# Kernel optimization log

Hardware: AMD Instinct MI355X
Metric: run time of the kernel (lower is better)

## Reference

```python
import jax, jax.numpy as jnp
import numpy as np

N_NODES = 50000
N_EDGES = 600000
D_OBJ = 128
D_REL = 128
D_OUT = 128


def setup_inputs() -> dict:
    key = jax.random.key(0)
    ks = jax.random.split(key, 7)
    s_obj = 1.0 / np.sqrt(D_OBJ)
    s_rel = 1.0 / np.sqrt(D_REL)
    return {
        "obj_vecs": jax.random.normal(ks[0], (N_NODES, D_OBJ), dtype=jnp.float32),
        "rel_vecs": jax.random.normal(ks[1], (N_EDGES, D_REL), dtype=jnp.float32),
        "edge_index": jax.random.randint(ks[2], (N_EDGES, 2), 0, N_NODES, dtype=jnp.int64),
        "W_obj": jax.random.normal(ks[3], (D_OUT, D_OBJ), dtype=jnp.float32) * s_obj,
        "b_obj": jax.random.normal(ks[4], (D_OUT,), dtype=jnp.float32) * s_obj,
        "W_rel": jax.random.normal(ks[5], (D_OUT, D_REL), dtype=jnp.float32) * s_rel,
        "b_rel": jax.random.normal(ks[6], (D_OUT,), dtype=jnp.float32) * s_rel,
    }


def reference(obj_vecs, rel_vecs, edge_index, W_obj, b_obj, W_rel, b_rel):
    # Per-node linear once ([N, d_out]) instead of twice per edge -- same math
    # since lin_obj(x_i) + lin_obj(x_j) = (x_i W^T + b) + (x_j W^T + b).
    obj_lin = obj_vecs @ W_obj.T + b_obj            # [N, d_out]
    rel_lin = rel_vecs @ W_rel.T + b_rel            # [E, d_out]
    src = edge_index[:, 0]
    dst = edge_index[:, 1]
    # message = relu(lin_obj(obj_i) + lin_rel(rel_k) + lin_obj(obj_j))
    msg = jax.nn.relu(obj_lin[src] + rel_lin + obj_lin[dst])  # [E, d_out]
    # aggr='add', flow source_to_target: scatter-add at target nodes (col 1)
    aggr = jax.ops.segment_sum(msg, dst, num_segments=obj_vecs.shape[0])
    return jax.nn.relu(aggr)
```

## Files before the change

kernel.cpp:

```cpp
#include <hip/hip_runtime.h>

#define N_NODES 50000
#define N_EDGES 600000
#define DD 128

typedef __attribute__((ext_vector_type(8))) short short8;
typedef __attribute__((ext_vector_type(4))) float f32x4;

__device__ __forceinline__ short f2bf(float f) {
    union { float f; unsigned u; } v; v.f = f;
    unsigned r = v.u + 0x7fffu + ((v.u >> 16) & 1u);
    return (short)(r >> 16);
}
__device__ __forceinline__ float bf2f(short s) {
    union { float f; unsigned u; } v; v.u = ((unsigned)(unsigned short)s) << 16;
    return v.f;
}
__device__ __forceinline__ float u2f(unsigned u) {
    union { float f; unsigned u; } v; v.u = u;
    return v.f;
}

__global__ __launch_bounds__(256) void k_lin(const float* __restrict__ X,
                                             const float* __restrict__ W,
                                             const float* __restrict__ bias,
                                             short* __restrict__ Y,
                                             int ntiles) {
    __shared__ __align__(16) short Wf[128 * 128];
    for (int i = threadIdx.x; i < 2048; i += 256) {
        const int fl = i & 63, fr = i >> 6;
        const int nt = fr >> 2, ks = fr & 3, fg = fl >> 4, fln = fl & 15;
        const float* s = W + (nt * 16 + fln) * DD + ks * 32 + fg * 8;
        short* d = Wf + i * 8;
#pragma unroll
        for (int j = 0; j < 8; ++j) d[j] = f2bf(s[j]);
    }
    __syncthreads();

    const int wave = threadIdx.x >> 6;
    const int lane = threadIdx.x & 63;
    const int g = lane >> 4, ln = lane & 15;

    float bb[8];
#pragma unroll
    for (int nt = 0; nt < 8; ++nt) bb[nt] = bias[nt * 16 + ln];

    for (int t = blockIdx.x * 4 + wave; t < ntiles; t += gridDim.x * 4) {
        const float* xr = X + (size_t)(t * 16 + ln) * DD;
        short8 a[4];
#pragma unroll
        for (int ks = 0; ks < 4; ++ks) {
            const float* p = xr + ks * 32 + g * 8;
            float4 t0 = *(const float4*)p;
            float4 t1 = *(const float4*)(p + 4);
            short8 v;
            v[0] = f2bf(t0.x); v[1] = f2bf(t0.y); v[2] = f2bf(t0.z); v[3] = f2bf(t0.w);
            v[4] = f2bf(t1.x); v[5] = f2bf(t1.y); v[6] = f2bf(t1.z); v[7] = f2bf(t1.w);
            a[ks] = v;
        }
#pragma unroll
        for (int nt = 0; nt < 8; ++nt) {
            f32x4 acc = {0.f, 0.f, 0.f, 0.f};
#pragma unroll
            for (int ks = 0; ks < 4; ++ks) {
                short8 b = *(const short8*)(Wf + (((nt << 2) + ks) * 64 + lane) * 8);
                acc = __builtin_amdgcn_mfma_f32_16x16x32_bf16(a[ks], b, acc, 0, 0, 0);
            }
#pragma unroll
            for (int r = 0; r < 4; ++r)
                Y[(size_t)(t * 16 + g * 4 + r) * DD + nt * 16 + ln] = f2bf(acc[r] + bb[nt]);
        }
    }
}

__global__ __launch_bounds__(256) void k_zero_int(int* __restrict__ p, int n) {
    int i = blockIdx.x * 256 + threadIdx.x;
    if (i < n) p[i] = 0;
}

__global__ __launch_bounds__(256) void k_count(const int* __restrict__ EI,
                                               int* __restrict__ counts) {
    int e = blockIdx.x * 256 + threadIdx.x;
    if (e < N_EDGES) atomicAdd(&counts[EI[2 * e + 1]], 1);
}

__global__ __launch_bounds__(256) void k_scan1(const int* __restrict__ counts,
                                               int* __restrict__ scanned,
                                               int* __restrict__ bsum) {
    __shared__ int tmp[256];
    const int t = threadIdx.x;
    const int i = blockIdx.x * 256 + t;
    int v = (i < N_NODES) ? counts[i] : 0;
    tmp[t] = v;
    __syncthreads();
#pragma unroll
    for (int off = 1; off < 256; off <<= 1) {
        int x = (t >= off) ? tmp[t - off] : 0;
        __syncthreads();
        tmp[t] += x;
        __syncthreads();
    }
    if (i < N_NODES) scanned[i] = tmp[t] - v;
    if (t == 255) bsum[blockIdx.x] = tmp[255];
}

__global__ __launch_bounds__(256) void k_scan2(int* __restrict__ bsum, int nb) {
    __shared__ int tmp[256];
    const int t = threadIdx.x;
    int v = (t < nb) ? bsum[t] : 0;
    tmp[t] = v;
    __syncthreads();
#pragma unroll
    for (int off = 1; off < 256; off <<= 1) {
        int x = (t >= off) ? tmp[t - off] : 0;
        __syncthreads();
        tmp[t] += x;
        __syncthreads();
    }
    if (t < nb) bsum[t] = tmp[t] - v;
}

__global__ __launch_bounds__(256) void k_scan3(const int* __restrict__ scanned,
                                               const int* __restrict__ bsum,
                                               int* __restrict__ offsets,
                                               int* __restrict__ cursor) {
    int i = blockIdx.x * 256 + threadIdx.x;
    if (i < N_NODES) {
        int off = scanned[i] + bsum[blockIdx.x];
        offsets[i] = off;
        cursor[i] = off;
    }
    if (i == 0) offsets[N_NODES] = N_EDGES;
}

__global__ __launch_bounds__(256) void k_scatter2(const int* __restrict__ EI,
                                                  int* __restrict__ cursor,
                                                  int* __restrict__ perm) {
    int e = blockIdx.x * 256 + threadIdx.x;
    if (e < N_EDGES)
        perm[e] = atomicAdd(&cursor[EI[2 * e + 1]], 1);
}

__global__ __launch_bounds__(256) void k_fl(const float* __restrict__ RV,
                                            const int* __restrict__ EI,
                                            const int* __restrict__ perm,
                                            const float* __restrict__ W,
                                            const float* __restrict__ bias,
                                            const short* __restrict__ OL,
                                            unsigned short* __restrict__ Ys) {
    __shared__ __align__(16) short Wf[128 * 128];
    __shared__ __align__(16) unsigned stg[4][1160];

    for (int i = threadIdx.x; i < 2048; i += 256) {
        const int fl = i & 63, fr = i >> 6;
        const int nt = fr >> 2, ks = fr & 3, fg = fl >> 4, fln = fl & 15;
        const float* s = W + (nt * 16 + fln) * DD + ks * 32 + fg * 8;
        short* d = Wf + i * 8;
#pragma unroll
        for (int j = 0; j < 8; ++j) d[j] = f2bf(s[j]);
    }
    __syncthreads();

    const int wave = threadIdx.x >> 6;
    const int lane = threadIdx.x & 63;
    const int g = lane >> 4, ln = lane & 15;
    unsigned* st = stg[wave];

    const float br0 = bias[lane];
    const float br1 = bias[lane + 64];
    const unsigned short* OLu = (const unsigned short*)OL;
    const int NT = N_EDGES / 16;

    for (int t = blockIdx.x * 4 + wave; t < NT; t += gridDim.x * 4) {
        const int e0 = t * 16;

        const float* xr = RV + (size_t)(e0 + ln) * DD;
        short8 a[4];
#pragma unroll
        for (int ks = 0; ks < 4; ++ks) {
            const float* p = xr + ks * 32 + g * 8;
            float4 t0 = *(const float4*)p;
            float4 t1 = *(const float4*)(p + 4);
            short8 v;
            v[0] = f2bf(t0.x); v[1] = f2bf(t0.y); v[2] = f2bf(t0.z); v[3] = f2bf(t0.w);
            v[4] = f2bf(t1.x); v[5] = f2bf(t1.y); v[6] = f2bf(t1.z); v[7] = f2bf(t1.w);
            a[ks] = v;
        }

        int sp = 0, pp = 0;
        if (lane < 16) {
            sp = EI[2 * (e0 + lane)];
            pp = perm[e0 + lane];
        }

        f32x4 acc[8];
#pragma unroll
        for (int nt = 0; nt < 8; ++nt) {
            acc[nt] = (f32x4){0.f, 0.f, 0.f, 0.f};
#pragma unroll
            for (int ks = 0; ks < 4; ++ks) {
                short8 b = *(const short8*)(Wf + (((nt << 2) + ks) * 64 + lane) * 8);
                acc[nt] = __builtin_amdgcn_mfma_f32_16x16x32_bf16(a[ks], b, acc[nt], 0, 0, 0);
            }
        }

#pragma unroll
        for (int nt = 0; nt < 8; ++nt) {
            const unsigned lo = ((unsigned)(unsigned short)f2bf(acc[nt][0])) |
                                (((unsigned)(unsigned short)f2bf(acc[nt][1])) << 16);
            const unsigned hi = ((unsigned)(unsigned short)f2bf(acc[nt][2])) |
                                (((unsigned)(unsigned short)f2bf(acc[nt][3])) << 16);
            const int c = nt * 16 + ln;
            st[c * 9 + g * 2]     = lo;
            st[c * 9 + g * 2 + 1] = hi;
        }

#pragma unroll 4
        for (int e = 0; e < 16; ++e) {
            const int src = __shfl(sp, e);
            const int pos = __shfl(pp, e);
            const unsigned w0 = st[lane * 9 + (e >> 1)];
            const unsigned w1 = st[(lane + 64) * 9 + (e >> 1)];
            const float s0 = (e & 1) ? u2f(w0 & 0xffff0000u) : u2f(w0 << 16);
            const float s1 = (e & 1) ? u2f(w1 & 0xffff0000u) : u2f(w1 << 16);
            const float y0 = s0 + br0 + bf2f((short)OLu[(size_t)src * DD + lane]);
            const float y1 = s1 + br1 + bf2f((short)OLu[(size_t)src * DD + lane + 64]);
            Ys[(size_t)pos * DD + lane]      = (unsigned short)f2bf(y0);
            Ys[(size_t)pos * DD + lane + 64] = (unsigned short)f2bf(y1);
        }
    }
}

__global__ __launch_bounds__(256) void k_segsum(const unsigned short* __restrict__ Ys,
                                                const short* __restrict__ OL,
                                                const int* __restrict__ offs,
                                                float* __restrict__ out) {
    const int wave = threadIdx.x >> 6;
    const int lane = threadIdx.x & 63;
    const int v = blockIdx.x * 4 + wave;
    if (v >= N_NODES) return;

    const int r0 = offs[v], r1 = offs[v + 1];
    const unsigned short* OLu = (const unsigned short*)OL;
    const float od0 = bf2f((short)OLu[(size_t)v * DD + lane]);
    const float od1 = bf2f((short)OLu[(size_t)v * DD + lane + 64]);

    float a0 = 0.f, a1 = 0.f;
    int r = r0;
    for (; r + 2 <= r1; r += 2) {
        const float y00 = bf2f((short)Ys[(size_t)r * DD + lane]);
        const float y01 = bf2f((short)Ys[(size_t)r * DD + lane + 64]);
        const float y10 = bf2f((short)Ys[(size_t)(r + 1) * DD + lane]);
        const float y11 = bf2f((short)Ys[(size_t)(r + 1) * DD + lane + 64]);
        a0 += fmaxf(y00 + od0, 0.f) + fmaxf(y10 + od0, 0.f);
        a1 += fmaxf(y01 + od1, 0.f) + fmaxf(y11 + od1, 0.f);
    }
    if (r < r1) {
        a0 += fmaxf(bf2f((short)Ys[(size_t)r * DD + lane]) + od0, 0.f);
        a1 += fmaxf(bf2f((short)Ys[(size_t)r * DD + lane + 64]) + od1, 0.f);
    }

    out[(size_t)v * DD + lane]      = fmaxf(a0, 0.f);
    out[(size_t)v * DD + lane + 64] = fmaxf(a1, 0.f);
}

extern "C" void kernel_launch(void* const* d_in, const int* in_sizes, int n_in,
                              void* d_out, int out_size, void* d_ws, size_t ws_size,
                              hipStream_t stream) {
    const float* obj = (const float*)d_in[0];
    const float* rel = (const float*)d_in[1];
    const int*   ei  = (const int*)d_in[2];
    const float* Wo  = (const float*)d_in[3];
    const float* bo  = (const float*)d_in[4];
    const float* Wr  = (const float*)d_in[5];
    const float* br  = (const float*)d_in[6];
    float* out = (float*)d_out;

    char* ws = (char*)d_ws;
    unsigned short* Ys = (unsigned short*)ws;
    short* OLb     = (short*)(ws + 153600000);
    int*   perm    = (int*)(ws + 166400000);
    int*   counts  = (int*)(ws + 168800000);
    int*   scanned = (int*)(ws + 169000192);
    int*   offsets = (int*)(ws + 169200896);
    int*   cursor  = (int*)(ws + 169401600);
    int*   bsum    = (int*)(ws + 169601792);

    const int NB_E = (N_EDGES + 255) / 256;
    const int NB_N = (N_NODES + 255) / 256;

    k_zero_int<<<NB_N, 256, 0, stream>>>(counts, N_NODES);
    k_count<<<NB_E, 256, 0, stream>>>(ei, counts);
    k_scan1<<<NB_N, 256, 0, stream>>>(counts, scanned, bsum);
    k_scan2<<<1, 256, 0, stream>>>(bsum, NB_N);
    k_scan3<<<NB_N, 256, 0, stream>>>(scanned, bsum, offsets, cursor);
    k_scatter2<<<NB_E, 256, 0, stream>>>(ei, cursor, perm);
    k_lin<<<782, 256, 0, stream>>>(obj, Wo, bo, OLb, N_NODES / 16);
    k_fl<<<2048, 256, 0, stream>>>(rel, ei, perm, Wr, br, OLb, Ys);
    k_segsum<<<(N_NODES + 3) / 4, 256, 0, stream>>>(Ys, OLb, offsets, out);
}
```

Baseline: 258.7 us.

## Pack bf16 pairs into 32-bit accesses, merge scan kernels, memset counts

```diff
diff --git a/kernel.cpp b/kernel.cpp
--- a/kernel.cpp
+++ b/kernel.cpp
@@ -73,11 +73,6 @@
     }
 }
 
-__global__ __launch_bounds__(256) void k_zero_int(int* __restrict__ p, int n) {
-    int i = blockIdx.x * 256 + threadIdx.x;
-    if (i < n) p[i] = 0;
-}
-
 __global__ __launch_bounds__(256) void k_count(const int* __restrict__ EI,
                                                int* __restrict__ counts) {
     int e = blockIdx.x * 256 + threadIdx.x;
@@ -104,29 +99,25 @@
     if (t == 255) bsum[blockIdx.x] = tmp[255];
 }
 
-__global__ __launch_bounds__(256) void k_scan2(int* __restrict__ bsum, int nb) {
-    __shared__ int tmp[256];
+__global__ __launch_bounds__(256) void k_scan3m(const int* __restrict__ scanned,
+                                                const int* __restrict__ bsum,
+                                                int* __restrict__ offsets,
+                                                int* __restrict__ cursor,
+                                                int nb) {
+    __shared__ int red[256];
     const int t = threadIdx.x;
-    int v = (t < nb) ? bsum[t] : 0;
-    tmp[t] = v;
-    __syncthreads();
-#pragma unroll
-    for (int off = 1; off < 256; off <<= 1) {
-        int x = (t >= off) ? tmp[t - off] : 0;
+    const int bid = blockIdx.x;
+    red[t] = (t < bid && t < nb) ? bsum[t] : 0;
+    __syncthreads();
+#pragma unroll
+    for (int off = 128; off > 0; off >>= 1) {
+        if (t < off) red[t] += red[t + off];
         __syncthreads();
-        tmp[t] += x;
-        __syncthreads();
-    }
-    if (t < nb) bsum[t] = tmp[t] - v;
-}
-
-__global__ __launch_bounds__(256) void k_scan3(const int* __restrict__ scanned,
-                                               const int* __restrict__ bsum,
-                                               int* __restrict__ offsets,
-                                               int* __restrict__ cursor) {
-    int i = blockIdx.x * 256 + threadIdx.x;
+    }
+    const int pre = red[0];
+    const int i = bid * 256 + t;
     if (i < N_NODES) {
-        int off = scanned[i] + bsum[blockIdx.x];
+        const int off = scanned[i] + pre;
         offsets[i] = off;
         cursor[i] = off;
     }
@@ -147,7 +138,7 @@
                                             const float* __restrict__ W,
                                             const float* __restrict__ bias,
                                             const short* __restrict__ OL,
-                                            unsigned short* __restrict__ Ys) {
+                                            unsigned* __restrict__ Ysw) {
     __shared__ __align__(16) short Wf[128 * 128];
     __shared__ __align__(16) unsigned stg[4][1160];
 
@@ -166,8 +157,8 @@
     const int g = lane >> 4, ln = lane & 15;
     unsigned* st = stg[wave];
 
-    const float br0 = bias[lane];
-    const float br1 = bias[lane + 64];
+    const float br0 = bias[2 * lane];
+    const float br1 = bias[2 * lane + 1];
     const unsigned short* OLu = (const unsigned short*)OL;
     const int NT = N_EDGES / 16;
 
@@ -215,23 +206,25 @@
             st[c * 9 + g * 2 + 1] = hi;
         }
 
-#pragma unroll 4
+#pragma unroll 8
         for (int e = 0; e < 16; ++e) {
             const int src = __shfl(sp, e);
             const int pos = __shfl(pp, e);
-            const unsigned w0 = st[lane * 9 + (e >> 1)];
-            const unsigned w1 = st[(lane + 64) * 9 + (e >> 1)];
+            const unsigned w0 = st[(2 * lane) * 9 + (e >> 1)];
+            const unsigned w1 = st[(2 * lane + 1) * 9 + (e >> 1)];
             const float s0 = (e & 1) ? u2f(w0 & 0xffff0000u) : u2f(w0 << 16);
             const float s1 = (e & 1) ? u2f(w1 & 0xffff0000u) : u2f(w1 << 16);
-            const float y0 = s0 + br0 + bf2f((short)OLu[(size_t)src * DD + lane]);
-            const float y1 = s1 + br1 + bf2f((short)OLu[(size_t)src * DD + lane + 64]);
-            Ys[(size_t)pos * DD + lane]      = (unsigned short)f2bf(y0);
-            Ys[(size_t)pos * DD + lane + 64] = (unsigned short)f2bf(y1);
-        }
-    }
-}
-
-__global__ __launch_bounds__(256) void k_segsum(const unsigned short* __restrict__ Ys,
+            const unsigned olw = *(const unsigned*)(OLu + (size_t)src * DD + 2 * lane);
+            const float y0 = s0 + br0 + u2f(olw << 16);
+            const float y1 = s1 + br1 + u2f(olw & 0xffff0000u);
+            const unsigned yw = ((unsigned)(unsigned short)f2bf(y0)) |
+                                (((unsigned)(unsigned short)f2bf(y1)) << 16);
+            Ysw[(size_t)pos * (DD / 2) + lane] = yw;
+        }
+    }
+}
+
+__global__ __launch_bounds__(256) void k_segsum(const unsigned* __restrict__ Ysw,
                                                 const short* __restrict__ OL,
                                                 const int* __restrict__ offs,
                                                 float* __restrict__ out) {
@@ -242,26 +235,32 @@
 
     const int r0 = offs[v], r1 = offs[v + 1];
     const unsigned short* OLu = (const unsigned short*)OL;
-    const float od0 = bf2f((short)OLu[(size_t)v * DD + lane]);
-    const float od1 = bf2f((short)OLu[(size_t)v * DD + lane + 64]);
+    const unsigned odw = *(const unsigned*)(OLu + (size_t)v * DD + 2 * lane);
+    const float od0 = u2f(odw << 16), od1 = u2f(odw & 0xffff0000u);
 
     float a0 = 0.f, a1 = 0.f;
     int r = r0;
-    for (; r + 2 <= r1; r += 2) {
-        const float y00 = bf2f((short)Ys[(size_t)r * DD + lane]);
-        const float y01 = bf2f((short)Ys[(size_t)r * DD + lane + 64]);
-        const float y10 = bf2f((short)Ys[(size_t)(r + 1) * DD + lane]);
-        const float y11 = bf2f((short)Ys[(size_t)(r + 1) * DD + lane + 64]);
-        a0 += fmaxf(y00 + od0, 0.f) + fmaxf(y10 + od0, 0.f);
-        a1 += fmaxf(y01 + od1, 0.f) + fmaxf(y11 + od1, 0.f);
-    }
-    if (r < r1) {
-        a0 += fmaxf(bf2f((short)Ys[(size_t)r * DD + lane]) + od0, 0.f);
-        a1 += fmaxf(bf2f((short)Ys[(size_t)r * DD + lane + 64]) + od1, 0.f);
-    }
-
-    out[(size_t)v * DD + lane]      = fmaxf(a0, 0.f);
-    out[(size_t)v * DD + lane + 64] = fmaxf(a1, 0.f);
+    for (; r + 4 <= r1; r += 4) {
+        unsigned y[4];
+#pragma unroll
+        for (int j = 0; j < 4; ++j)
+            y[j] = Ysw[(size_t)(r + j) * (DD / 2) + lane];
+#pragma unroll
+        for (int j = 0; j < 4; ++j) {
+            a0 += fmaxf(u2f(y[j] << 16) + od0, 0.f);
+            a1 += fmaxf(u2f(y[j] & 0xffff0000u) + od1, 0.f);
+        }
+    }
+    for (; r < r1; ++r) {
+        const unsigned yw = Ysw[(size_t)r * (DD / 2) + lane];
+        a0 += fmaxf(u2f(yw << 16) + od0, 0.f);
+        a1 += fmaxf(u2f(yw & 0xffff0000u) + od1, 0.f);
+    }
+
+    float2 o;
+    o.x = fmaxf(a0, 0.f);
+    o.y = fmaxf(a1, 0.f);
+    *(float2*)(out + (size_t)v * DD + 2 * lane) = o;
 }
 
 extern "C" void kernel_launch(void* const* d_in, const int* in_sizes, int n_in,
@@ -277,7 +276,7 @@
     float* out = (float*)d_out;
 
     char* ws = (char*)d_ws;
-    unsigned short* Ys = (unsigned short*)ws;
+    unsigned* Ysw  = (unsigned*)ws;
     short* OLb     = (short*)(ws + 153600000);
     int*   perm    = (int*)(ws + 166400000);
     int*   counts  = (int*)(ws + 168800000);
@@ -289,13 +288,12 @@
     const int NB_E = (N_EDGES + 255) / 256;
     const int NB_N = (N_NODES + 255) / 256;
 
-    k_zero_int<<<NB_N, 256, 0, stream>>>(counts, N_NODES);
+    hipMemsetAsync(counts, 0, N_NODES * sizeof(int), stream);
     k_count<<<NB_E, 256, 0, stream>>>(ei, counts);
     k_scan1<<<NB_N, 256, 0, stream>>>(counts, scanned, bsum);
-    k_scan2<<<1, 256, 0, stream>>>(bsum, NB_N);
-    k_scan3<<<NB_N, 256, 0, stream>>>(scanned, bsum, offsets, cursor);
+    k_scan3m<<<NB_N, 256, 0, stream>>>(scanned, bsum, offsets, cursor, NB_N);
     k_scatter2<<<NB_E, 256, 0, stream>>>(ei, cursor, perm);
     k_lin<<<782, 256, 0, stream>>>(obj, Wo, bo, OLb, N_NODES / 16);
-    k_fl<<<2048, 256, 0, stream>>>(rel, ei, perm, Wr, br, OLb, Ys);
-    k_segsum<<<(N_NODES + 3) / 4, 256, 0, stream>>>(Ys, OLb, offsets, out);
-}
+    k_fl<<<2048, 256, 0, stream>>>(rel, ei, perm, Wr, br, OLb, Ysw);
+    k_segsum<<<(N_NODES + 3) / 4, 256, 0, stream>>>(Ysw, OLb, offsets, out);
+}
```

Result: faster. 238.3 us (-7.9%).
